# Kernel optimization log

Measured on AMD Instinct MI355X. Metric: run time of the kernel, lower is better.

Reference implementation:

```python
import jax, jax.numpy as jnp
import numpy as np

T = 4096
HID = 64          # hidden size (hard-coded 64 in forward)
EMB = 8           # direction embed size
NA = 7            # num actions
CONV_OUT = 64 * 15 * 15   # 64x64 input -> 31x31 -> 15x15, 64 channels
RIN = CONV_OUT + EMB      # GRU input size = 14408


def setup_inputs() -> dict:
    key = jax.random.key(0)
    ks = jax.random.split(key, 16)
    s = 0.05
    return {
        "image": jax.random.uniform(ks[0], (T, 1, 64, 64, 3), dtype=jnp.float32) * 255.0,
        "direction": jax.random.randint(ks[1], (T, 1), 0, 4),
        "conv1_w": jax.random.normal(ks[2], (32, 3, 3, 3), dtype=jnp.float32) * s,
        "conv1_b": jax.random.normal(ks[3], (32,), dtype=jnp.float32) * s,
        "conv2_w": jax.random.normal(ks[4], (64, 32, 3, 3), dtype=jnp.float32) * s,
        "conv2_b": jax.random.normal(ks[5], (64,), dtype=jnp.float32) * s,
        "emb": jax.random.normal(ks[6], (4, EMB), dtype=jnp.float32) * s,
        "w_ih": jax.random.normal(ks[7], (3 * HID, RIN), dtype=jnp.float32) * s,
        "b_ih": jax.random.normal(ks[8], (3 * HID,), dtype=jnp.float32) * s,
        "w_hh": jax.random.normal(ks[9], (3 * HID, HID), dtype=jnp.float32) * s,
        "b_hh": jax.random.normal(ks[10], (3 * HID,), dtype=jnp.float32) * s,
        "actor_w": jax.random.normal(ks[11], (NA, HID), dtype=jnp.float32) * s,
        "actor_b": jax.random.normal(ks[12], (NA,), dtype=jnp.float32) * s,
        "critic_w": jax.random.normal(ks[13], (1, HID), dtype=jnp.float32) * s,
        "critic_b": jax.random.normal(ks[14], (1,), dtype=jnp.float32) * s,
    }


def _conv(x, w, b):
    y = jax.lax.conv_general_dilated(x, w, (2, 2), 'VALID',
                                     dimension_numbers=('NCHW', 'OIHW', 'NCHW'))
    return jax.nn.relu(y + b[None, :, None, None])


def reference(image, direction, conv1_w, conv1_b, conv2_w, conv2_b, emb,
              w_ih, b_ih, w_hh, b_hh, actor_w, actor_b, critic_w, critic_b):
    img = image[:, 0]              # [T,H,W,3]  (squeeze env-batch dim)
    d = direction[:, 0]            # [T]
    x = (img / 255.0).transpose(0, 3, 1, 2)        # NCHW [T,3,64,64]
    x = _conv(x, conv1_w, conv1_b)                 # [T,32,31,31]
    x = _conv(x, conv2_w, conv2_b)                 # [T,64,15,15]
    conv_out = x.reshape(x.shape[0], -1)           # [T,14400] (C,H,W order == torch Flatten)
    feat = jnp.concatenate([conv_out, emb[d]], axis=1)   # [T,RIN]

    # Precompute input-side gate projections for all timesteps in one GEMM
    gx = feat @ w_ih.T + b_ih                      # [T,3H]

    def step(h, gx_t):
        gh = h @ w_hh.T + b_hh                     # [3H]
        r = jax.nn.sigmoid(gx_t[:HID] + gh[:HID])
        z = jax.nn.sigmoid(gx_t[HID:2*HID] + gh[HID:2*HID])
        n = jnp.tanh(gx_t[2*HID:] + r * gh[2*HID:])
        h_new = (1.0 - z) * n + z * h
        return h_new, h_new

    _, hs = jax.lax.scan(step, jnp.zeros((HID,), dtype=feat.dtype), gx)  # [T,HID]

    logits = hs @ actor_w.T + actor_b              # [T,NA]
    values = (hs @ critic_w.T + critic_b)[:, 0]    # [T]
    policy = jax.nn.softmax(logits, axis=-1)
    return policy, values
```

## Files before the change

### kernel.cpp

```cpp
#include <hip/hip_runtime.h>

#define T_STEPS 4096
#define HID 64
#define FEAT_LD 14464
#define SPLITK 8

typedef unsigned int uint;
typedef unsigned short ushort_t;
typedef _Float16 h2v __attribute__((ext_vector_type(2)));
typedef _Float16 v8h __attribute__((ext_vector_type(8)));
typedef float v4f __attribute__((ext_vector_type(4)));

__device__ __forceinline__ uint cvtpk(float a, float b) {
  return __builtin_bit_cast(uint, __builtin_amdgcn_cvt_pkrtz(a, b));
}
__device__ __forceinline__ uint packrelu(float a, float b) {
  return __builtin_bit_cast(
      uint, __builtin_amdgcn_cvt_pkrtz(fmaxf(a, 0.f), fmaxf(b, 0.f)));
}

__global__ __launch_bounds__(256) void prep_b(const float* __restrict__ w_ih,
                                              _Float16* __restrict__ Bw) {
  int i = blockIdx.x * 256 + threadIdx.x;
  if (i >= 192 * FEAT_LD) return;
  int row = i / FEAT_LD, col = i - row * FEAT_LD;
  Bw[i] = (col < 14408) ? (_Float16)w_ih[row * 14408 + col] : (_Float16)0.f;
}

__global__ __launch_bounds__(256) void prep_conv(const float* __restrict__ w1,
                                                 const float* __restrict__ w2,
                                                 _Float16* __restrict__ bpack1,
                                                 _Float16* __restrict__ bpack) {
  int t = blockIdx.x * 256 + threadIdx.x;
  if (t < 2048) {
    int j = t & 7, l = (t >> 3) & 63, nf = (t >> 9) & 1, ks = t >> 10;
    int k = ks * 32 + ((l >> 4) * 8) + j;
    int cc = k & 3, kk = k >> 2;
    int oc = nf * 16 + (l & 15);
    float v = (cc < 3 && kk < 9) ? w1[oc * 27 + cc * 9 + kk] : 0.f;
    bpack1[t] = (_Float16)v;
  }
  if (t < 18432) {
    int j = t & 7, l = (t >> 3) & 63, nf = (t >> 9) & 3, kk = t >> 11;
    int oc = nf * 16 + (l & 15), ic = (l >> 4) * 8 + j;
    bpack[t] = (_Float16)w2[oc * 288 + ic * 9 + kk];
  }
}

__global__ __launch_bounds__(256, 5) void conv_kernel(
    const float* __restrict__ image, const int* __restrict__ dir,
    const _Float16* __restrict__ bpack1, const float* __restrict__ b1,
    const _Float16* __restrict__ bpack, const float* __restrict__ b2,
    const float* __restrict__ emb, _Float16* __restrict__ feat, int imgBase) {
  __shared__ __align__(16) _Float16 img_s[1216 * 4];
  __shared__ __align__(16) char c1_s[288 * 64];

  ushort_t* out_s = (ushort_t*)img_s;

  const int tid = threadIdx.x;
  const int wid = tid >> 6, lane = tid & 63;
  const int lrow = lane & 15, lq = lane >> 4;
  const int qh = blockIdx.x;
  const int img = imgBase + blockIdx.y;
  const int q3 = (qh == 3);
  const int nrows = q3 ? 16 : 19;
  const int nvalid = q3 ? 217 : 279;
  const int npos = q3 ? 45 : 60;
  const float* ip = image + (size_t)img * 12288 + (size_t)qh * 16 * 192;
  _Float16* fr = feat + (size_t)blockIdx.y * FEAT_LD;

  const float kn = 1.f / 255.f;
  const int ng = nrows * 16;
  for (int g = tid; g < ng; g += 256) {
    const float* s0 = ip + g * 12;
    float4 A = *(const float4*)s0, B = *(const float4*)(s0 + 4),
           C = *(const float4*)(s0 + 8);
    uint4 u0, u1;
    u0.x = cvtpk(A.x * kn, A.y * kn);
    u0.y = cvtpk(A.z * kn, 0.f);
    u0.z = cvtpk(A.w * kn, B.x * kn);
    u0.w = cvtpk(B.y * kn, 0.f);
    u1.x = cvtpk(B.z * kn, B.w * kn);
    u1.y = cvtpk(C.x * kn, 0.f);
    u1.z = cvtpk(C.y * kn, C.z * kn);
    u1.w = cvtpk(C.w * kn, 0.f);
    *(uint4*)(img_s + g * 16) = u0;
    *(uint4*)(img_s + g * 16 + 8) = u1;
  }
  if (qh == 0 && tid < 64) {
    int d = dir[img];
    fr[14400 + tid] = (tid < 8) ? (_Float16)emb[d * 8 + tid] : (_Float16)0.f;
  }

  v8h bw1[2][2];
#pragma unroll
  for (int nf = 0; nf < 2; ++nf)
#pragma unroll
    for (int ks = 0; ks < 2; ++ks)
      bw1[nf][ks] =
          *(const v8h*)(bpack1 + ((size_t)(ks * 2 + nf) * 64 + lane) * 8);
  const float4 b1q0 = *(const float4*)(b1 + lq * 4);
  const float4 b1q1 = *(const float4*)(b1 + 16 + lq * 4);

  const int kk0 = 2 * lq, kk1 = 2 * lq + 1;
  const int off0 = ((kk0 / 3) * 64 + (kk0 - 3 * (kk0 / 3))) * 4;
  const int off1 = ((kk1 / 3) * 64 + (kk1 - 3 * (kk1 / 3))) * 4;
  const int off8 = (2 * 64 + 2) * 4;
  __syncthreads();

#pragma unroll
  for (int f = 0; f < 5; ++f) {
    const int mf = wid + 4 * f;
    if (mf >= 18) break;
    const int pin = mf * 16 + lrow;
    const int pv = (pin < 279) ? pin : 278;
    const int ly = pv / 31, lx = pv - 31 * ly;
    const _Float16* pb = img_s + ((2 * ly) * 64 + 2 * lx) * 4;
    uint2 p0 = *(const uint2*)(pb + off0);
    uint2 p1 = *(const uint2*)(pb + off1);
    uint2 p8 = *(const uint2*)(pb + off8);
    uint4 u0;
    u0.x = p0.x; u0.y = p0.y; u0.z = p1.x; u0.w = p1.y;
    uint4 u1;
    u1.x = (lq == 0) ? p8.x : 0u;
    u1.y = (lq == 0) ? p8.y : 0u;
    u1.z = 0u; u1.w = 0u;
    v8h a0 = __builtin_bit_cast(v8h, u0);
    v8h a1 = __builtin_bit_cast(v8h, u1);
    v4f ac0 = __builtin_bit_cast(v4f, b1q0);
    v4f ac1 = __builtin_bit_cast(v4f, b1q1);
    ac0 = __builtin_amdgcn_mfma_f32_16x16x32_f16(bw1[0][0], a0, ac0, 0, 0, 0);
    ac0 = __builtin_amdgcn_mfma_f32_16x16x32_f16(bw1[0][1], a1, ac0, 0, 0, 0);
    ac1 = __builtin_amdgcn_mfma_f32_16x16x32_f16(bw1[1][0], a0, ac1, 0, 0, 0);
    ac1 = __builtin_amdgcn_mfma_f32_16x16x32_f16(bw1[1][1], a1, ac1, 0, 0, 0);
    if (pin < nvalid) {
      char* base = c1_s + pin * 64;
      const int sw = (pin >> 1) & 3;
      uint2 u;
      u.x = packrelu(ac0[0], ac0[1]);
      u.y = packrelu(ac0[2], ac0[3]);
      *(uint2*)(base + ((((lq >> 1) ^ sw) << 4) + (lq & 1) * 8)) = u;
      u.x = packrelu(ac1[0], ac1[1]);
      u.y = packrelu(ac1[2], ac1[3]);
      *(uint2*)(base + ((((2 + (lq >> 1)) ^ sw) << 4) + (lq & 1) * 8)) = u;
    }
  }
  __syncthreads();

  const int pos = wid * 16 + lrow;
  const int pv2 = (pos < npos) ? pos : 0;
  const int oy = pv2 / 15, ox = pv2 - 15 * oy;
  const int abase = (2 * oy) * 31 + 2 * ox;
  v4f acc[4];
#pragma unroll
  for (int nf = 0; nf < 4; ++nf) {
    float bv = b2[nf * 16 + lrow];
    acc[nf] = (v4f){bv, bv, bv, bv};
  }
  v8h bcur[4];
#pragma unroll
  for (int nf = 0; nf < 4; ++nf)
    bcur[nf] = *(const v8h*)(bpack + ((size_t)nf * 64 + lane) * 8);
#pragma unroll
  for (int kk = 0; kk < 9; ++kk) {
    v8h bnxt[4];
    if (kk < 8) {
#pragma unroll
      for (int nf = 0; nf < 4; ++nf)
        bnxt[nf] =
            *(const v8h*)(bpack + ((size_t)((kk + 1) * 4 + nf) * 64 + lane) * 8);
    }
    const int dd = (kk / 3) * 31 + (kk - 3 * (kk / 3));
    const int pin = abase + dd;
    const int sw = (pin >> 1) & 3;
    v8h af = *(const v8h*)(c1_s + pin * 64 + ((lq ^ sw) << 4));
#pragma unroll
    for (int nf = 0; nf < 4; ++nf)
      acc[nf] =
          __builtin_amdgcn_mfma_f32_16x16x32_f16(af, bcur[nf], acc[nf], 0, 0, 0);
    if (kk < 8) {
#pragma unroll
      for (int nf = 0; nf < 4; ++nf) bcur[nf] = bnxt[nf];
    }
  }
  __syncthreads();
  {
    const int p0 = wid * 16 + lq * 4;
#pragma unroll
    for (int nf = 0; nf < 4; ++nf) {
      int oc = nf * 16 + lrow;
      uint2 u;
      u.x = packrelu(acc[nf][0], acc[nf][1]);
      u.y = packrelu(acc[nf][2], acc[nf][3]);
      *(uint2*)(out_s + oc * 64 + p0) = u;
    }
  }
  __syncthreads();
  {
    ushort_t* fru = (ushort_t*)fr;
    const int basep = 60 * qh;
    for (int i = tid; i < 4096; i += 256) {
      int oc = i >> 6, pp = i & 63;
      if (pp < npos) fru[oc * 225 + basep + pp] = out_s[oc * 64 + pp];
    }
  }
}

__global__ __launch_bounds__(256, 2) void gemm_kernel(
    const _Float16* __restrict__ feat, const _Float16* __restrict__ Bw,
    float* __restrict__ gxp, int rowBase, int mt) {
  __shared__ __align__(16) _Float16 As[2][64 * 64];
  __shared__ __align__(16) _Float16 Bs[2][192 * 64];
  const int tid = threadIdx.x;
  const int w = tid >> 6, lane = tid & 63;
  const int lrow = lane & 15, lq = lane >> 4;

  const int nwg = mt * SPLITK;
  const int q = nwg >> 3, r = nwg & 7;
  const int xcd = blockIdx.x & 7, pos = blockIdx.x >> 3;
  const int wg = (xcd < r ? xcd * (q + 1) : r * (q + 1) + (xcd - r) * q) + pos;
  const int sk = wg / mt, m = wg - sk * mt;
  const int bm = m * 64;
  const int ks0 = (sk * 226) / SPLITK, ks1 = ((sk + 1) * 226) / SPLITK;

  int rowA[2], kcA[2], offA[2], rowB[6], kcB[6], offB[6];
#pragma unroll
  for (int i = 0; i < 2; ++i) {
    int s = w * 128 + i * 64 + lane;
    rowA[i] = s >> 3;
    kcA[i] = s & 7;
    offA[i] = rowA[i] * 128 + ((kcA[i] ^ (rowA[i] & 7)) << 4);
  }
#pragma unroll
  for (int i = 0; i < 6; ++i) {
    int s = w * 384 + i * 64 + lane;
    rowB[i] = s >> 3;
    kcB[i] = s & 7;
    offB[i] = rowB[i] * 128 + ((kcB[i] ^ (rowB[i] & 7)) << 4);
  }

  uint4 ta[2], tb[6];
  {
    int kb = ks0 * 64;
#pragma unroll
    for (int i = 0; i < 2; ++i)
      ta[i] = *(const uint4*)(feat + (size_t)(bm + rowA[i]) * FEAT_LD + kb +
                              kcA[i] * 8);
#pragma unroll
    for (int i = 0; i < 6; ++i)
      tb[i] = *(const uint4*)(Bw + (size_t)rowB[i] * FEAT_LD + kb + kcB[i] * 8);
#pragma unroll
    for (int i = 0; i < 2; ++i) *(uint4*)((char*)As[0] + offA[i]) = ta[i];
#pragma unroll
    for (int i = 0; i < 6; ++i) *(uint4*)((char*)Bs[0] + offB[i]) = tb[i];
  }
  __syncthreads();

  v4f acc[4][3] = {};
  for (int ks = ks0; ks < ks1; ++ks) {
    const int cur = (ks - ks0) & 1;
    const bool more = (ks + 1 < ks1);
    if (more) {
      int kb = (ks + 1) * 64;
#pragma unroll
      for (int i = 0; i < 2; ++i)
        ta[i] = *(const uint4*)(feat + (size_t)(bm + rowA[i]) * FEAT_LD + kb +
                                kcA[i] * 8);
#pragma unroll
      for (int i = 0; i < 6; ++i)
        tb[i] =
            *(const uint4*)(Bw + (size_t)rowB[i] * FEAT_LD + kb + kcB[i] * 8);
    }
    const char* Ab = (const char*)As[cur];
    const char* Bb = (const char*)Bs[cur];
#pragma unroll
    for (int ksub = 0; ksub < 2; ++ksub) {
      int s0 = ksub * 4 + lq;
      v8h afr[4];
#pragma unroll
      for (int mf = 0; mf < 4; ++mf) {
        int row = mf * 16 + lrow;
        afr[mf] = *(const v8h*)(Ab + row * 128 + ((s0 ^ (row & 7)) << 4));
      }
#pragma unroll
      for (int nfi = 0; nfi < 3; ++nfi) {
        int col = (w * 3 + nfi) * 16 + lrow;
        v8h bfr = *(const v8h*)(Bb + col * 128 + ((s0 ^ (col & 7)) << 4));
#pragma unroll
        for (int mf = 0; mf < 4; ++mf)
          acc[mf][nfi] = __builtin_amdgcn_mfma_f32_16x16x32_f16(
              afr[mf], bfr, acc[mf][nfi], 0, 0, 0);
      }
    }
    if (more) {
      char* An = (char*)As[cur ^ 1];
      char* Bn = (char*)Bs[cur ^ 1];
#pragma unroll
      for (int i = 0; i < 2; ++i) *(uint4*)(An + offA[i]) = ta[i];
#pragma unroll
      for (int i = 0; i < 6; ++i) *(uint4*)(Bn + offB[i]) = tb[i];
    }
    __syncthreads();
  }
  const size_t obase = (size_t)sk * T_STEPS;
#pragma unroll
  for (int mf = 0; mf < 4; ++mf) {
#pragma unroll
    for (int nfi = 0; nfi < 3; ++nfi) {
      int col = (w * 3 + nfi) * 16 + lrow;
#pragma unroll
      for (int qq = 0; qq < 4; ++qq) {
        int rowm = bm + mf * 16 + lq * 4 + qq;
        gxp[(obase + rowBase + rowm) * 192 + col] = acc[mf][nfi][qq];
      }
    }
  }
}

__global__ __launch_bounds__(256) void reduce_gx(const float* __restrict__ gxp,
                                                 const float* __restrict__ b_ih,
                                                 float* __restrict__ gx) {
  int t = blockIdx.x * 256 + threadIdx.x;
  if (t >= T_STEPS * 192) return;
  int col = t - (t / 192) * 192;
  float s = b_ih[col];
#pragma unroll
  for (int k = 0; k < SPLITK; ++k) s += gxp[(size_t)k * T_STEPS * 192 + t];
  gx[t] = s;
}

__global__ __launch_bounds__(192) void scan_kernel(
    const float* __restrict__ gx, const float* __restrict__ w_hh,
    const float* __restrict__ b_hh, float* __restrict__ hs, int C, int W) {
  __shared__ __align__(16) float h_s[64];
  __shared__ float r_s[64], z_s[64];
  const int tid = threadIdx.x;
  const int g = tid >> 6, j = tid & 63;
  const int b = blockIdx.x;
  const int tstore = b * C;
  const int t0 = max(0, tstore - W);
  const int t1 = tstore + C;

  float w[64];
#pragma unroll
  for (int k4 = 0; k4 < 16; ++k4) {
    float4 v = *(const float4*)(w_hh + tid * 64 + k4 * 4);
    w[4 * k4 + 0] = v.x;
    w[4 * k4 + 1] = v.y;
    w[4 * k4 + 2] = v.z;
    w[4 * k4 + 3] = v.w;
  }
  const float bh = b_hh[tid];
  if (tid < 64) h_s[tid] = 0.f;
  __syncthreads();

  float gxv = gx[(size_t)t0 * 192 + tid];
  for (int t = t0; t < t1; ++t) {
    int tn = (t + 1 < T_STEPS) ? t + 1 : T_STEPS - 1;
    float gxn = gx[(size_t)tn * 192 + tid];
    float gacc0 = bh, gacc1 = 0.f, gacc2 = 0.f, gacc3 = 0.f;
#pragma unroll
    for (int k4 = 0; k4 < 4; ++k4) {
      float4 hA = *(const float4*)(h_s + 0 + k4 * 4);
      float4 hB = *(const float4*)(h_s + 16 + k4 * 4);
      float4 hC = *(const float4*)(h_s + 32 + k4 * 4);
      float4 hD = *(const float4*)(h_s + 48 + k4 * 4);
      gacc0 = fmaf(w[0 + 4 * k4], hA.x, gacc0);
      gacc0 = fmaf(w[1 + 4 * k4], hA.y, gacc0);
      gacc0 = fmaf(w[2 + 4 * k4], hA.z, gacc0);
      gacc0 = fmaf(w[3 + 4 * k4], hA.w, gacc0);
      gacc1 = fmaf(w[16 + 4 * k4], hB.x, gacc1);
      gacc1 = fmaf(w[17 + 4 * k4], hB.y, gacc1);
      gacc1 = fmaf(w[18 + 4 * k4], hB.z, gacc1);
      gacc1 = fmaf(w[19 + 4 * k4], hB.w, gacc1);
      gacc2 = fmaf(w[32 + 4 * k4], hC.x, gacc2);
      gacc2 = fmaf(w[33 + 4 * k4], hC.y, gacc2);
      gacc2 = fmaf(w[34 + 4 * k4], hC.z, gacc2);
      gacc2 = fmaf(w[35 + 4 * k4], hC.w, gacc2);
      gacc3 = fmaf(w[48 + 4 * k4], hD.x, gacc3);
      gacc3 = fmaf(w[49 + 4 * k4], hD.y, gacc3);
      gacc3 = fmaf(w[50 + 4 * k4], hD.z, gacc3);
      gacc3 = fmaf(w[51 + 4 * k4], hD.w, gacc3);
    }
    float gh = (gacc0 + gacc1) + (gacc2 + gacc3);
    if (g == 0)
      r_s[j] = 1.f / (1.f + __expf(-(gxv + gh)));
    else if (g == 1)
      z_s[j] = 1.f / (1.f + __expf(-(gxv + gh)));
    __syncthreads();
    if (g == 2) {
      float r = r_s[j], z = z_s[j];
      float x = gxv + r * gh;
      float x2 = fminf(fmaxf(2.f * x, -30.f), 30.f);
      float e = __expf(x2);
      float n = (e - 1.f) / (e + 1.f);
      float hn = (1.f - z) * n + z * h_s[j];
      h_s[j] = hn;
      if (t >= tstore) hs[(size_t)t * 64 + j] = hn;
    }
    __syncthreads();
    gxv = gxn;
  }
}

__global__ __launch_bounds__(256) void head_kernel(
    const float* __restrict__ hs, const float* __restrict__ aw,
    const float* __restrict__ ab, const float* __restrict__ cw,
    const float* __restrict__ cb, float* __restrict__ out) {
  int t = blockIdx.x * 256 + threadIdx.x;
  if (t >= T_STEPS) return;
  float h[64];
#pragma unroll
  for (int i = 0; i < 16; ++i) {
    float4 v = *(const float4*)(hs + (size_t)t * 64 + 4 * i);
    h[4 * i + 0] = v.x;
    h[4 * i + 1] = v.y;
    h[4 * i + 2] = v.z;
    h[4 * i + 3] = v.w;
  }
  float lg[7];
#pragma unroll
  for (int o = 0; o < 7; ++o) {
    float a = ab[o];
#pragma unroll
    for (int jj = 0; jj < 64; ++jj) a = fmaf(aw[o * 64 + jj], h[jj], a);
    lg[o] = a;
  }
  float v = cb[0];
#pragma unroll
  for (int jj = 0; jj < 64; ++jj) v = fmaf(cw[jj], h[jj], v);
  float m = lg[0];
#pragma unroll
  for (int o = 1; o < 7; ++o) m = fmaxf(m, lg[o]);
  float e[7], s = 0.f;
#pragma unroll
  for (int o = 0; o < 7; ++o) {
    e[o] = __expf(lg[o] - m);
    s += e[o];
  }
  float inv = 1.f / s;
#pragma unroll
  for (int o = 0; o < 7; ++o) out[(size_t)t * 7 + o] = e[o] * inv;
  out[(size_t)T_STEPS * 7 + t] = v;
}

extern "C" void kernel_launch(void* const* d_in, const int* in_sizes, int n_in,
                              void* d_out, int out_size, void* d_ws,
                              size_t ws_size, hipStream_t stream) {
  const float* image = (const float*)d_in[0];
  const int* dir = (const int*)d_in[1];
  const float* w1 = (const float*)d_in[2];
  const float* b1 = (const float*)d_in[3];
  const float* w2 = (const float*)d_in[4];
  const float* b2 = (const float*)d_in[5];
  const float* emb = (const float*)d_in[6];
  const float* w_ih = (const float*)d_in[7];
  const float* b_ih = (const float*)d_in[8];
  const float* w_hh = (const float*)d_in[9];
  const float* b_hh = (const float*)d_in[10];
  const float* aw = (const float*)d_in[11];
  const float* ab = (const float*)d_in[12];
  const float* cw = (const float*)d_in[13];
  const float* cb = (const float*)d_in[14];
  float* out = (float*)d_out;

  const size_t bp1Bytes = 4096;
  const size_t bpackBytes = 18432 * 2;
  const size_t bBytes = (size_t)192 * FEAT_LD * 2;
  const size_t gxpBytes = (size_t)SPLITK * T_STEPS * 192 * 4;
  const size_t gxBytes = (size_t)T_STEPS * 192 * 4;
  const size_t hsBytes = (size_t)T_STEPS * 64 * 4;
  const size_t fixed =
      bp1Bytes + bpackBytes + bBytes + gxpBytes + gxBytes + hsBytes;
  int CH = 4096;
  while (CH > 256 && fixed + (size_t)CH * FEAT_LD * 2 > ws_size) CH >>= 1;

  char* p = (char*)d_ws;
  _Float16* bpack1 = (_Float16*)p;
  p += bp1Bytes;
  _Float16* bpack = (_Float16*)p;
  p += bpackBytes;
  _Float16* Bw = (_Float16*)p;
  p += bBytes;
  float* gxp = (float*)p;
  p += gxpBytes;
  float* gx = (float*)p;
  p += gxBytes;
  float* hs = (float*)p;
  p += hsBytes;
  _Float16* featBuf = (_Float16*)p;

  prep_conv<<<72, 256, 0, stream>>>(w1, w2, bpack1, bpack);
  prep_b<<<(192 * FEAT_LD + 255) / 256, 256, 0, stream>>>(w_ih, Bw);
  for (int c = 0; c < T_STEPS; c += CH) {
    conv_kernel<<<dim3(4, CH), 256, 0, stream>>>(image, dir, bpack1, b1, bpack,
                                                 b2, emb, featBuf, c);
    gemm_kernel<<<(CH / 64) * SPLITK, 256, 0, stream>>>(featBuf, Bw, gxp, c,
                                                        CH / 64);
  }
  reduce_gx<<<(T_STEPS * 192 + 255) / 256, 256, 0, stream>>>(gxp, b_ih, gx);
  scan_kernel<<<256, 192, 0, stream>>>(gx, w_hh, b_hh, hs, 16, 160);
  head_kernel<<<(T_STEPS + 255) / 256, 256, 0, stream>>>(hs, aw, ab, cw, cb,
                                                         out);
}
```

Baseline: 423.9 us.

## Double conv kernel block to 512 threads and split conv2 output channels across waves

The conv kernel now launches 8 waves per block instead of 4. The conv1 stage strides its m-fragments over 8 waves, and each conv2 wave handles one position fragment and two of the four output-channel fragments, which halves per-wave MFMA work and accumulator registers. The conv1 output in LDS is re-laid out so even and odd positions sit in separate halves, intended to reduce bank conflicts for the stride-2 reads in conv2. The cost is that each wave now loads the same A fragment redundantly for its channel pair, and the block has more threads to synchronise.

```diff
diff --git a/kernel.cpp b/kernel.cpp
--- a/kernel.cpp
+++ b/kernel.cpp
@@ -47,7 +47,7 @@
   }
 }
 
-__global__ __launch_bounds__(256, 5) void conv_kernel(
+__global__ __launch_bounds__(512, 8) void conv_kernel(
     const float* __restrict__ image, const int* __restrict__ dir,
     const _Float16* __restrict__ bpack1, const float* __restrict__ b1,
     const _Float16* __restrict__ bpack, const float* __restrict__ b2,
@@ -71,7 +71,7 @@
 
   const float kn = 1.f / 255.f;
   const int ng = nrows * 16;
-  for (int g = tid; g < ng; g += 256) {
+  for (int g = tid; g < ng; g += 512) {
     const float* s0 = ip + g * 12;
     float4 A = *(const float4*)s0, B = *(const float4*)(s0 + 4),
            C = *(const float4*)(s0 + 8);
@@ -109,8 +109,8 @@
   __syncthreads();
 
 #pragma unroll
-  for (int f = 0; f < 5; ++f) {
-    const int mf = wid + 4 * f;
+  for (int f = 0; f < 3; ++f) {
+    const int mf = wid + 8 * f;
     if (mf >= 18) break;
     const int pin = mf * 16 + lrow;
     const int pv = (pin < 279) ? pin : 278;
@@ -134,7 +134,7 @@
     ac1 = __builtin_amdgcn_mfma_f32_16x16x32_f16(bw1[1][0], a0, ac1, 0, 0, 0);
     ac1 = __builtin_amdgcn_mfma_f32_16x16x32_f16(bw1[1][1], a1, ac1, 0, 0, 0);
     if (pin < nvalid) {
-      char* base = c1_s + pin * 64;
+      char* base = c1_s + ((pin & 1) * 144 + (pin >> 1)) * 64;
       const int sw = (pin >> 1) & 3;
       uint2 u;
       u.x = packrelu(ac0[0], ac0[1]);
@@ -147,51 +147,53 @@
   }
   __syncthreads();
 
-  const int pos = wid * 16 + lrow;
+  const int mfw = wid >> 1, nfb = (wid & 1) * 2;
+  const int pos = mfw * 16 + lrow;
   const int pv2 = (pos < npos) ? pos : 0;
   const int oy = pv2 / 15, ox = pv2 - 15 * oy;
   const int abase = (2 * oy) * 31 + 2 * ox;
-  v4f acc[4];
-#pragma unroll
-  for (int nf = 0; nf < 4; ++nf) {
-    float bv = b2[nf * 16 + lrow];
-    acc[nf] = (v4f){bv, bv, bv, bv};
-  }
-  v8h bcur[4];
-#pragma unroll
-  for (int nf = 0; nf < 4; ++nf)
-    bcur[nf] = *(const v8h*)(bpack + ((size_t)nf * 64 + lane) * 8);
+  v4f acc[2];
+#pragma unroll
+  for (int i = 0; i < 2; ++i) {
+    float bv = b2[(nfb + i) * 16 + lrow];
+    acc[i] = (v4f){bv, bv, bv, bv};
+  }
+  v8h bcur[2];
+#pragma unroll
+  for (int i = 0; i < 2; ++i)
+    bcur[i] = *(const v8h*)(bpack + ((size_t)(nfb + i) * 64 + lane) * 8);
 #pragma unroll
   for (int kk = 0; kk < 9; ++kk) {
-    v8h bnxt[4];
+    v8h bnxt[2];
     if (kk < 8) {
 #pragma unroll
-      for (int nf = 0; nf < 4; ++nf)
-        bnxt[nf] =
-            *(const v8h*)(bpack + ((size_t)((kk + 1) * 4 + nf) * 64 + lane) * 8);
+      for (int i = 0; i < 2; ++i)
+        bnxt[i] = *(const v8h*)(bpack +
+                                ((size_t)((kk + 1) * 4 + nfb + i) * 64 + lane) * 8);
     }
     const int dd = (kk / 3) * 31 + (kk - 3 * (kk / 3));
     const int pin = abase + dd;
     const int sw = (pin >> 1) & 3;
-    v8h af = *(const v8h*)(c1_s + pin * 64 + ((lq ^ sw) << 4));
-#pragma unroll
-    for (int nf = 0; nf < 4; ++nf)
-      acc[nf] =
-          __builtin_amdgcn_mfma_f32_16x16x32_f16(af, bcur[nf], acc[nf], 0, 0, 0);
+    const char* base = c1_s + ((pin & 1) * 144 + (pin >> 1)) * 64;
+    v8h af = *(const v8h*)(base + ((lq ^ sw) << 4));
+#pragma unroll
+    for (int i = 0; i < 2; ++i)
+      acc[i] =
+          __builtin_amdgcn_mfma_f32_16x16x32_f16(af, bcur[i], acc[i], 0, 0, 0);
     if (kk < 8) {
 #pragma unroll
-      for (int nf = 0; nf < 4; ++nf) bcur[nf] = bnxt[nf];
+      for (int i = 0; i < 2; ++i) bcur[i] = bnxt[i];
     }
   }
   __syncthreads();
   {
-    const int p0 = wid * 16 + lq * 4;
-#pragma unroll
-    for (int nf = 0; nf < 4; ++nf) {
-      int oc = nf * 16 + lrow;
+    const int p0 = mfw * 16 + lq * 4;
+#pragma unroll
+    for (int i = 0; i < 2; ++i) {
+      int oc = (nfb + i) * 16 + lrow;
       uint2 u;
-      u.x = packrelu(acc[nf][0], acc[nf][1]);
-      u.y = packrelu(acc[nf][2], acc[nf][3]);
+      u.x = packrelu(acc[i][0], acc[i][1]);
+      u.y = packrelu(acc[i][2], acc[i][3]);
       *(uint2*)(out_s + oc * 64 + p0) = u;
     }
   }
@@ -199,7 +201,7 @@
   {
     ushort_t* fru = (ushort_t*)fr;
     const int basep = 60 * qh;
-    for (int i = tid; i < 4096; i += 256) {
+    for (int i = tid; i < 4096; i += 512) {
       int oc = i >> 6, pp = i & 63;
       if (pp < npos) fru[oc * 225 + basep + pp] = out_s[oc * 64 + pp];
     }
@@ -493,7 +495,7 @@
   prep_conv<<<72, 256, 0, stream>>>(w1, w2, bpack1, bpack);
   prep_b<<<(192 * FEAT_LD + 255) / 256, 256, 0, stream>>>(w_ih, Bw);
   for (int c = 0; c < T_STEPS; c += CH) {
-    conv_kernel<<<dim3(4, CH), 256, 0, stream>>>(image, dir, bpack1, b1, bpack,
+    conv_kernel<<<dim3(4, CH), 512, 0, stream>>>(image, dir, bpack1, b1, bpack,
                                                  b2, emb, featBuf, c);
     gemm_kernel<<<(CH / 64) * SPLITK, 256, 0, stream>>>(featBuf, Bw, gxp, c,
                                                         CH / 64);
```

Result: no change. 418.3 us (-1.3%).
